# Performance work log

Measured on AMD Instinct MI355X. Metric: run time of the kernel, lower is better.

## Reference

```python
import jax, jax.numpy as jnp
import numpy as np
import math

B_CH = 128   # bottleneck channels (conv1x1 in)
N_CH = 256   # encoder filters (conv1x1 out / linear in)
L = 16       # filter length (linear out); hop = L//2
BATCH = 8
K = 32000    # number of frames
T_ORIGIN = (L // 2) * (K - 1) + L  # 256008


def setup_inputs() -> dict:
    key = jax.random.key(0)
    k1, k2, k3, k4 = jax.random.split(key, 4)
    return {
        "mixture_w": jax.random.normal(k1, (BATCH, N_CH, K), jnp.float32),
        "est_mask": jax.random.normal(k2, (BATCH, B_CH, K), jnp.float32),
        "W_mask": jax.random.normal(k3, (N_CH, B_CH), jnp.float32) * (1.0 / np.sqrt(B_CH)),
        "W_basis": jax.random.normal(k4, (L, N_CH), jnp.float32) * (1.0 / np.sqrt(N_CH)),
        "T_origin": T_ORIGIN,
    }


def overlap_and_add(signal, frame_step):
    # signal: [..., frames, frame_length]
    frames, frame_length = signal.shape[-2], signal.shape[-1]
    sub_len = math.gcd(frame_length, frame_step)
    sub_step = frame_step // sub_len
    spf = frame_length // sub_len  # subframes per frame
    out_size = frame_step * (frames - 1) + frame_length
    out_sub = out_size // sub_len
    sub_sig = signal.reshape(signal.shape[:-2] + (frames * spf, sub_len))
    # scatter index for each subframe (same as torch unfold + index_add_)
    idx = (jnp.arange(frames)[:, None] * sub_step + jnp.arange(spf)[None, :]).reshape(-1)
    res = jnp.zeros(signal.shape[:-2] + (out_sub, sub_len), signal.dtype)
    res = res.at[..., idx, :].add(sub_sig)
    return res.reshape(signal.shape[:-2] + (out_size,))


def reference(mixture_w, est_mask, W_mask, W_basis, T_origin):
    # conv1x1 (bias-free) == channel matmul: [B_CH -> N_CH]
    m = jnp.einsum('nb,gbk->gnk', W_mask, est_mask)   # [batch, N, K]
    x = mixture_w * jax.nn.relu(m)                    # masked encoder output
    # transpose + Linear(N -> L, no bias): [batch, K, L]
    x = jnp.einsum('gnk,ln->gkl', x, W_basis)
    est_source = overlap_and_add(x, L // 2)           # [batch, T_conv]
    pad = T_origin - est_source.shape[-1]
    return jnp.pad(est_source, ((0, 0), (0, pad)))
```

## Files before the change

### kernel.cpp

```cpp
#include <hip/hip_runtime.h>
#include <stdint.h>

#define BATCH 8
#define NCH 256
#define BCH 128
#define KFR 32000
#define TOUT 256008
#define KT 32
#define NCHUNK (KFR / KT)
#define ESTW 64
#define XTW 128
#define LOC_FLOATS (8 * KT + 8)

typedef __attribute__((ext_vector_type(8))) short bf16x8;
typedef __attribute__((ext_vector_type(4))) float f32x4;

__device__ __forceinline__ unsigned short f32_to_bf16(float f) {
    unsigned int u = __builtin_bit_cast(unsigned int, f);
    u += 0x7FFFu + ((u >> 16) & 1u);
    return (unsigned short)(u >> 16);
}
__device__ __forceinline__ unsigned int pack2(float a, float b) {
    return (unsigned int)f32_to_bf16(a) | ((unsigned int)f32_to_bf16(b) << 16);
}
__device__ __forceinline__ int swz(int row, int w) {
    return (((w >> 2) ^ (((row >> 2) & 3) << 1)) << 2) | (w & 3);
}

__global__ void convert_weights(const float* __restrict__ Wm,
                                const float* __restrict__ Wb,
                                unsigned short* __restrict__ wbf) {
    int i = blockIdx.x * 256 + threadIdx.x;
    if (i < NCH * BCH) wbf[i] = f32_to_bf16(Wm[i]);
    if (i < 16 * NCH)  wbf[NCH * BCH + i] = f32_to_bf16(Wb[i]);
}

__global__ __launch_bounds__(256, 4)
void fused_decoder(const float* __restrict__ mix,
                   const float* __restrict__ est,
                   const unsigned short* __restrict__ wbf,
                   float* __restrict__ out) {
    __shared__ __align__(16) unsigned int estd[32 * ESTW];
    __shared__ __align__(16) unsigned int xtd[32 * XTW];
    __shared__ __align__(16) float locout[LOC_FLOATS];

    const int tid = threadIdx.x;
    const int lane = tid & 63;
    const int wv = tid >> 6;
    const int l15 = lane & 15;
    const int lq = lane >> 4;
    const int f4 = tid & 7;
    const int c0 = tid >> 3;

    const int bid = blockIdx.x;
    const int g = bid / NCHUNK;
    const int c = bid % NCHUNK;
    const int k0 = c * KT;

    if (tid < LOC_FLOATS / 4) {
        f32x4 z = {0.f, 0.f, 0.f, 0.f};
        *reinterpret_cast<f32x4*>(locout + 4 * tid) = z;
    }

    const float* eg = est + ((size_t)g * BCH) * KFR + k0;
    const float* mg = mix + ((size_t)g * NCH) * KFR + k0;

    {
        f32x4 e0 = *reinterpret_cast<const f32x4*>(eg + (size_t)(2 * c0) * KFR + 4 * f4);
        f32x4 e1 = *reinterpret_cast<const f32x4*>(eg + (size_t)(2 * c0 + 1) * KFR + 4 * f4);
        f32x4 e2 = *reinterpret_cast<const f32x4*>(eg + (size_t)(2 * c0 + 64) * KFR + 4 * f4);
        f32x4 e3 = *reinterpret_cast<const f32x4*>(eg + (size_t)(2 * c0 + 65) * KFR + 4 * f4);
#pragma unroll
        for (int i = 0; i < 4; ++i) {
            int row = 4 * f4 + i;
            estd[row * ESTW + swz(row, c0)]      = pack2(e0[i], e1[i]);
            estd[row * ESTW + swz(row, c0 + 32)] = pack2(e2[i], e3[i]);
        }
    }
    __syncthreads();

    {
        unsigned short* xts = reinterpret_cast<unsigned short*>(xtd);
#pragma unroll
        for (int nt = 0; nt < 4; ++nt) {
            const int n = 64 * wv + 16 * nt + l15;
            const unsigned short* wr = wbf + n * BCH + 8 * lq;
            bf16x8 w0 = *reinterpret_cast<const bf16x8*>(wr);
            bf16x8 w1 = *reinterpret_cast<const bf16x8*>(wr + 32);
            bf16x8 w2 = *reinterpret_cast<const bf16x8*>(wr + 64);
            bf16x8 w3 = *reinterpret_cast<const bf16x8*>(wr + 96);
#pragma unroll
            for (int ft = 0; ft < 2; ++ft) {
                const int fA = 16 * ft + l15;
                const int sgA = ((l15 >> 2) & 3) << 1;
                const unsigned int* br = estd + fA * ESTW;
                bf16x8 a0 = *reinterpret_cast<const bf16x8*>(br + (((0  + lq) ^ sgA) << 2));
                bf16x8 a1 = *reinterpret_cast<const bf16x8*>(br + (((4  + lq) ^ sgA) << 2));
                bf16x8 a2 = *reinterpret_cast<const bf16x8*>(br + (((8  + lq) ^ sgA) << 2));
                bf16x8 a3 = *reinterpret_cast<const bf16x8*>(br + (((12 + lq) ^ sgA) << 2));
                f32x4 a = {0.f, 0.f, 0.f, 0.f};
                a = __builtin_amdgcn_mfma_f32_16x16x32_bf16(a0, w0, a, 0, 0, 0);
                a = __builtin_amdgcn_mfma_f32_16x16x32_bf16(a1, w1, a, 0, 0, 0);
                a = __builtin_amdgcn_mfma_f32_16x16x32_bf16(a2, w2, a, 0, 0, 0);
                a = __builtin_amdgcn_mfma_f32_16x16x32_bf16(a3, w3, a, 0, 0, 0);
                const int f0 = 16 * ft + 4 * lq;
                f32x4 m = *reinterpret_cast<const f32x4*>(mg + (size_t)n * KFR + f0);
                float x0 = (a[0] > 0.f) ? m[0] * a[0] : 0.f;
                float x1 = (a[1] > 0.f) ? m[1] * a[1] : 0.f;
                float x2 = (a[2] > 0.f) ? m[2] * a[2] : 0.f;
                float x3 = (a[3] > 0.f) ? m[3] * a[3] : 0.f;
                const int swi = (((n >> 3) ^ (lq << 1)) << 2) | ((n >> 1) & 3);
                const int base = f0 * 256 + swi * 2 + (n & 1);
                xts[base]       = f32_to_bf16(x0);
                xts[base + 256] = f32_to_bf16(x1);
                xts[base + 512] = f32_to_bf16(x2);
                xts[base + 768] = f32_to_bf16(x3);
            }
        }
    }
    __syncthreads();

    if (wv < 2) {
        const int f = 16 * wv + l15;
        const int sg = ((f >> 2) & 3) << 1;
        const unsigned int* br = xtd + f * XTW;
        const unsigned short* wb2 = wbf + NCH * BCH + l15 * NCH + 8 * lq;
        f32x4 acc2 = {0.f, 0.f, 0.f, 0.f};
#pragma unroll
        for (int ks = 0; ks < 8; ++ks) {
            bf16x8 a = *reinterpret_cast<const bf16x8*>(wb2 + 32 * ks);
            bf16x8 b = *reinterpret_cast<const bf16x8*>(br + (((4 * ks + lq) ^ sg) << 2));
            acc2 = __builtin_amdgcn_mfma_f32_16x16x32_bf16(a, b, acc2, 0, 0, 0);
        }
        int src = (lane + 31) & 63;
        float p0 = __shfl(acc2[0], src, 64);
        float p1 = __shfl(acc2[1], src, 64);
        float p2 = __shfl(acc2[2], src, 64);
        float p3 = __shfl(acc2[3], src, 64);
        if (lq < 2) {
            int toff = 8 * f + 4 * lq;
            if (l15 == 0) {
                atomicAdd(locout + toff + 0, acc2[0]);
                atomicAdd(locout + toff + 1, acc2[1]);
                atomicAdd(locout + toff + 2, acc2[2]);
                atomicAdd(locout + toff + 3, acc2[3]);
            } else {
                f32x4 s = {acc2[0] + p0, acc2[1] + p1, acc2[2] + p2, acc2[3] + p3};
                *reinterpret_cast<f32x4*>(locout + toff) = s;
            }
        } else if (l15 == 15) {
            int toff = 8 * (16 * wv + 16) + 4 * (lq - 2);
            atomicAdd(locout + toff + 0, acc2[0]);
            atomicAdd(locout + toff + 1, acc2[1]);
            atomicAdd(locout + toff + 2, acc2[2]);
            atomicAdd(locout + toff + 3, acc2[3]);
        }
    }
    __syncthreads();

    if (tid < LOC_FLOATS / 4) {
        float* og = out + (size_t)g * TOUT + (size_t)(8 * KT) * c;
        f32x4 v = *reinterpret_cast<const f32x4*>(locout + 4 * tid);
        if (tid >= 2 && tid < (LOC_FLOATS / 4 - 2)) {
            *reinterpret_cast<f32x4*>(og + 4 * tid) = v;
        } else {
            atomicAdd(og + 4 * tid + 0, v[0]);
            atomicAdd(og + 4 * tid + 1, v[1]);
            atomicAdd(og + 4 * tid + 2, v[2]);
            atomicAdd(og + 4 * tid + 3, v[3]);
        }
    }
}

extern "C" void kernel_launch(void* const* d_in, const int* in_sizes, int n_in,
                              void* d_out, int out_size, void* d_ws, size_t ws_size,
                              hipStream_t stream) {
    const float* mix = (const float*)d_in[0];
    const float* est = (const float*)d_in[1];
    const float* Wm  = (const float*)d_in[2];
    const float* Wb  = (const float*)d_in[3];
    unsigned short* wbf = (unsigned short*)d_ws;

    hipMemsetAsync(d_out, 0, (size_t)out_size * sizeof(float), stream);
    convert_weights<<<128, 256, 0, stream>>>(Wm, Wb, wbf);
    fused_decoder<<<BATCH * NCHUNK, 256, 0, stream>>>(mix, est, wbf, (float*)d_out);
}
```

Baseline: 153.9 us.

## Prefetch mixture loads before first barrier and pad LDS rows

Moves all eight mixture_w global loads for each wave ahead of the est staging barrier so they run alongside the LDS fill and the first GEMM, instead of being issued inside the MFMA loop. Pads the LDS row strides (64→68, 128→132) to change the bank mapping, and relaxes launch bounds from 4 to 2 waves-per-EU to make room for the extra live registers. The cost is higher register pressure and possibly lower occupancy, and the padded strides may interact badly with the existing XOR swizzle.

```diff
diff --git a/kernel.cpp b/kernel.cpp
--- a/kernel.cpp
+++ b/kernel.cpp
@@ -8,8 +8,8 @@
 #define TOUT 256008
 #define KT 32
 #define NCHUNK (KFR / KT)
-#define ESTW 64
-#define XTW 128
+#define ESTW 68
+#define XTW 132
 #define LOC_FLOATS (8 * KT + 8)
 
 typedef __attribute__((ext_vector_type(8))) short bf16x8;
@@ -35,7 +35,39 @@
     if (i < 16 * NCH)  wbf[NCH * BCH + i] = f32_to_bf16(Wb[i]);
 }
 
-__global__ __launch_bounds__(256, 4)
+#define G1(NT, FT, MM) { \
+    const int n = 64 * wv + 16 * (NT) + l15; \
+    const unsigned short* wr = wbf + n * BCH + 8 * lq; \
+    bf16x8 w0 = *reinterpret_cast<const bf16x8*>(wr); \
+    bf16x8 w1 = *reinterpret_cast<const bf16x8*>(wr + 32); \
+    bf16x8 w2 = *reinterpret_cast<const bf16x8*>(wr + 64); \
+    bf16x8 w3 = *reinterpret_cast<const bf16x8*>(wr + 96); \
+    const int fA = 16 * (FT) + l15; \
+    const int sgA = ((l15 >> 2) & 3) << 1; \
+    const unsigned int* br = estd + fA * ESTW; \
+    bf16x8 a0 = *reinterpret_cast<const bf16x8*>(br + (((0  + lq) ^ sgA) << 2)); \
+    bf16x8 a1 = *reinterpret_cast<const bf16x8*>(br + (((4  + lq) ^ sgA) << 2)); \
+    bf16x8 a2 = *reinterpret_cast<const bf16x8*>(br + (((8  + lq) ^ sgA) << 2)); \
+    bf16x8 a3 = *reinterpret_cast<const bf16x8*>(br + (((12 + lq) ^ sgA) << 2)); \
+    f32x4 a = {0.f, 0.f, 0.f, 0.f}; \
+    a = __builtin_amdgcn_mfma_f32_16x16x32_bf16(a0, w0, a, 0, 0, 0); \
+    a = __builtin_amdgcn_mfma_f32_16x16x32_bf16(a1, w1, a, 0, 0, 0); \
+    a = __builtin_amdgcn_mfma_f32_16x16x32_bf16(a2, w2, a, 0, 0, 0); \
+    a = __builtin_amdgcn_mfma_f32_16x16x32_bf16(a3, w3, a, 0, 0, 0); \
+    float x0 = (a[0] > 0.f) ? (MM)[0] * a[0] : 0.f; \
+    float x1 = (a[1] > 0.f) ? (MM)[1] * a[1] : 0.f; \
+    float x2 = (a[2] > 0.f) ? (MM)[2] * a[2] : 0.f; \
+    float x3 = (a[3] > 0.f) ? (MM)[3] * a[3] : 0.f; \
+    const int f0 = 16 * (FT) + 4 * lq; \
+    const int swi = (((n >> 3) ^ (lq << 1)) << 2) | ((n >> 1) & 3); \
+    const int base = f0 * (2 * XTW) + swi * 2 + (n & 1); \
+    xts[base]               = f32_to_bf16(x0); \
+    xts[base + 2 * XTW]     = f32_to_bf16(x1); \
+    xts[base + 4 * XTW]     = f32_to_bf16(x2); \
+    xts[base + 6 * XTW]     = f32_to_bf16(x3); \
+}
+
+__global__ __launch_bounds__(256, 2)
 void fused_decoder(const float* __restrict__ mix,
                    const float* __restrict__ est,
                    const unsigned short* __restrict__ wbf,
@@ -65,58 +97,38 @@
     const float* eg = est + ((size_t)g * BCH) * KFR + k0;
     const float* mg = mix + ((size_t)g * NCH) * KFR + k0;
 
-    {
-        f32x4 e0 = *reinterpret_cast<const f32x4*>(eg + (size_t)(2 * c0) * KFR + 4 * f4);
-        f32x4 e1 = *reinterpret_cast<const f32x4*>(eg + (size_t)(2 * c0 + 1) * KFR + 4 * f4);
-        f32x4 e2 = *reinterpret_cast<const f32x4*>(eg + (size_t)(2 * c0 + 64) * KFR + 4 * f4);
-        f32x4 e3 = *reinterpret_cast<const f32x4*>(eg + (size_t)(2 * c0 + 65) * KFR + 4 * f4);
+    f32x4 e0 = *reinterpret_cast<const f32x4*>(eg + (size_t)(2 * c0) * KFR + 4 * f4);
+    f32x4 e1 = *reinterpret_cast<const f32x4*>(eg + (size_t)(2 * c0 + 1) * KFR + 4 * f4);
+    f32x4 e2 = *reinterpret_cast<const f32x4*>(eg + (size_t)(2 * c0 + 64) * KFR + 4 * f4);
+    f32x4 e3 = *reinterpret_cast<const f32x4*>(eg + (size_t)(2 * c0 + 65) * KFR + 4 * f4);
+    const float* pmb = mg + (size_t)(64 * wv + l15) * KFR + 4 * lq;
+    f32x4 m00 = *reinterpret_cast<const f32x4*>(pmb);
+    f32x4 m01 = *reinterpret_cast<const f32x4*>(pmb + 16);
+    f32x4 m10 = *reinterpret_cast<const f32x4*>(pmb + (size_t)16 * KFR);
+    f32x4 m11 = *reinterpret_cast<const f32x4*>(pmb + (size_t)16 * KFR + 16);
+    f32x4 m20 = *reinterpret_cast<const f32x4*>(pmb + (size_t)32 * KFR);
+    f32x4 m21 = *reinterpret_cast<const f32x4*>(pmb + (size_t)32 * KFR + 16);
+    f32x4 m30 = *reinterpret_cast<const f32x4*>(pmb + (size_t)48 * KFR);
+    f32x4 m31 = *reinterpret_cast<const f32x4*>(pmb + (size_t)48 * KFR + 16);
+
 #pragma unroll
-        for (int i = 0; i < 4; ++i) {
-            int row = 4 * f4 + i;
-            estd[row * ESTW + swz(row, c0)]      = pack2(e0[i], e1[i]);
-            estd[row * ESTW + swz(row, c0 + 32)] = pack2(e2[i], e3[i]);
-        }
+    for (int i = 0; i < 4; ++i) {
+        int row = 4 * f4 + i;
+        estd[row * ESTW + swz(row, c0)]      = pack2(e0[i], e1[i]);
+        estd[row * ESTW + swz(row, c0 + 32)] = pack2(e2[i], e3[i]);
     }
     __syncthreads();
 
     {
         unsigned short* xts = reinterpret_cast<unsigned short*>(xtd);
-#pragma unroll
-        for (int nt = 0; nt < 4; ++nt) {
-            const int n = 64 * wv + 16 * nt + l15;
-            const unsigned short* wr = wbf + n * BCH + 8 * lq;
-            bf16x8 w0 = *reinterpret_cast<const bf16x8*>(wr);
-            bf16x8 w1 = *reinterpret_cast<const bf16x8*>(wr + 32);
-            bf16x8 w2 = *reinterpret_cast<const bf16x8*>(wr + 64);
-            bf16x8 w3 = *reinterpret_cast<const bf16x8*>(wr + 96);
-#pragma unroll
-            for (int ft = 0; ft < 2; ++ft) {
-                const int fA = 16 * ft + l15;
-                const int sgA = ((l15 >> 2) & 3) << 1;
-                const unsigned int* br = estd + fA * ESTW;
-                bf16x8 a0 = *reinterpret_cast<const bf16x8*>(br + (((0  + lq) ^ sgA) << 2));
-                bf16x8 a1 = *reinterpret_cast<const bf16x8*>(br + (((4  + lq) ^ sgA) << 2));
-                bf16x8 a2 = *reinterpret_cast<const bf16x8*>(br + (((8  + lq) ^ sgA) << 2));
-                bf16x8 a3 = *reinterpret_cast<const bf16x8*>(br + (((12 + lq) ^ sgA) << 2));
-                f32x4 a = {0.f, 0.f, 0.f, 0.f};
-                a = __builtin_amdgcn_mfma_f32_16x16x32_bf16(a0, w0, a, 0, 0, 0);
-                a = __builtin_amdgcn_mfma_f32_16x16x32_bf16(a1, w1, a, 0, 0, 0);
-                a = __builtin_amdgcn_mfma_f32_16x16x32_bf16(a2, w2, a, 0, 0, 0);
-                a = __builtin_amdgcn_mfma_f32_16x16x32_bf16(a3, w3, a, 0, 0, 0);
-                const int f0 = 16 * ft + 4 * lq;
-                f32x4 m = *reinterpret_cast<const f32x4*>(mg + (size_t)n * KFR + f0);
-                float x0 = (a[0] > 0.f) ? m[0] * a[0] : 0.f;
-                float x1 = (a[1] > 0.f) ? m[1] * a[1] : 0.f;
-                float x2 = (a[2] > 0.f) ? m[2] * a[2] : 0.f;
-                float x3 = (a[3] > 0.f) ? m[3] * a[3] : 0.f;
-                const int swi = (((n >> 3) ^ (lq << 1)) << 2) | ((n >> 1) & 3);
-                const int base = f0 * 256 + swi * 2 + (n & 1);
-                xts[base]       = f32_to_bf16(x0);
-                xts[base + 256] = f32_to_bf16(x1);
-                xts[base + 512] = f32_to_bf16(x2);
-                xts[base + 768] = f32_to_bf16(x3);
-            }
-        }
+        G1(0, 0, m00)
+        G1(0, 1, m01)
+        G1(1, 0, m10)
+        G1(1, 1, m11)
+        G1(2, 0, m20)
+        G1(2, 1, m21)
+        G1(3, 0, m30)
+        G1(3, 1, m31)
     }
     __syncthreads();
 
```

New measurement: 144.6 us. 1.06x faster.

## Enlarge frame tile and stream mixture channels through LDS with software pipelining

Applied to the files above, without the earlier changes.

Each block now handles 128 frames instead of 32, so there are a quarter as many blocks and fewer boundary atomics. The 256 output channels are processed in eight 32-channel slices. Each slice of mixture data is staged through LDS, and the next slice is prefetched into registers while the current slice's conv and basis MFMAs run. The second GEMM accumulates across slices in registers instead of as a separate phase. In exchange, LDS use per block is higher, occupancy is halved through launch bounds, and there are two barriers per slice.

```diff
diff --git a/kernel.cpp b/kernel.cpp
--- a/kernel.cpp
+++ b/kernel.cpp
@@ -6,10 +6,11 @@
 #define BCH 128
 #define KFR 32000
 #define TOUT 256008
-#define KT 32
+#define KT 128
 #define NCHUNK (KFR / KT)
-#define ESTW 64
-#define XTW 128
+#define ESTW 68
+#define MIXW 132
+#define XTW2 20
 #define LOC_FLOATS (8 * KT + 8)
 
 typedef __attribute__((ext_vector_type(8))) short bf16x8;
@@ -35,139 +36,194 @@
     if (i < 16 * NCH)  wbf[NCH * BCH + i] = f32_to_bf16(Wb[i]);
 }
 
-__global__ __launch_bounds__(256, 4)
+__global__ __launch_bounds__(256, 2)
 void fused_decoder(const float* __restrict__ mix,
                    const float* __restrict__ est,
                    const unsigned short* __restrict__ wbf,
                    float* __restrict__ out) {
-    __shared__ __align__(16) unsigned int estd[32 * ESTW];
-    __shared__ __align__(16) unsigned int xtd[32 * XTW];
-    __shared__ __align__(16) float locout[LOC_FLOATS];
+    __shared__ __align__(16) unsigned int estd[128 * ESTW];
+    __shared__ __align__(16) float        mixs[32 * MIXW];
+    __shared__ __align__(16) unsigned int xtd[128 * XTW2];
+    __shared__ __align__(16) float        locout[1040];
 
     const int tid = threadIdx.x;
     const int lane = tid & 63;
     const int wv = tid >> 6;
     const int l15 = lane & 15;
     const int lq = lane >> 4;
+    const int l31 = lane & 31;
+    const int hi = lane >> 5;
     const int f4 = tid & 7;
     const int c0 = tid >> 3;
 
     const int bid = blockIdx.x;
     const int g = bid / NCHUNK;
     const int c = bid % NCHUNK;
-    const int k0 = c * KT;
-
-    if (tid < LOC_FLOATS / 4) {
+
+    const float* eg = est + ((size_t)g * BCH) * KFR + c * KT;
+    const float* mg = mix + ((size_t)g * NCH) * KFR + c * KT;
+
+    f32x4 e0, e1, e2, e3;
+    {
+        const float* p = eg + (size_t)(2 * c0) * KFR + 4 * f4;
+        e0 = *reinterpret_cast<const f32x4*>(p);
+        e1 = *reinterpret_cast<const f32x4*>(p + (size_t)KFR);
+        e2 = *reinterpret_cast<const f32x4*>(p + (size_t)64 * KFR);
+        e3 = *reinterpret_cast<const f32x4*>(p + (size_t)65 * KFR);
+    }
+    f32x4 mr0, mr1, mr2, mr3;
+    {
+        const float* p = mg + (size_t)(8 * wv + hi) * KFR + 4 * l31;
+        mr0 = *reinterpret_cast<const f32x4*>(p);
+        mr1 = *reinterpret_cast<const f32x4*>(p + (size_t)2 * KFR);
+        mr2 = *reinterpret_cast<const f32x4*>(p + (size_t)4 * KFR);
+        mr3 = *reinterpret_cast<const f32x4*>(p + (size_t)6 * KFR);
+    }
+
+    for (int t2 = tid; t2 < 260; t2 += 256) {
         f32x4 z = {0.f, 0.f, 0.f, 0.f};
-        *reinterpret_cast<f32x4*>(locout + 4 * tid) = z;
-    }
-
-    const float* eg = est + ((size_t)g * BCH) * KFR + k0;
-    const float* mg = mix + ((size_t)g * NCH) * KFR + k0;
-
-    {
-        f32x4 e0 = *reinterpret_cast<const f32x4*>(eg + (size_t)(2 * c0) * KFR + 4 * f4);
-        f32x4 e1 = *reinterpret_cast<const f32x4*>(eg + (size_t)(2 * c0 + 1) * KFR + 4 * f4);
-        f32x4 e2 = *reinterpret_cast<const f32x4*>(eg + (size_t)(2 * c0 + 64) * KFR + 4 * f4);
-        f32x4 e3 = *reinterpret_cast<const f32x4*>(eg + (size_t)(2 * c0 + 65) * KFR + 4 * f4);
+        *reinterpret_cast<f32x4*>(locout + 4 * t2) = z;
+    }
+
+#pragma unroll
+    for (int fb = 0; fb < 4; ++fb) {
 #pragma unroll
         for (int i = 0; i < 4; ++i) {
-            int row = 4 * f4 + i;
+            int row = 32 * fb + 4 * f4 + i;
             estd[row * ESTW + swz(row, c0)]      = pack2(e0[i], e1[i]);
             estd[row * ESTW + swz(row, c0 + 32)] = pack2(e2[i], e3[i]);
         }
+        if (fb < 3) {
+            const float* p = eg + (size_t)(2 * c0) * KFR + 32 * (fb + 1) + 4 * f4;
+            e0 = *reinterpret_cast<const f32x4*>(p);
+            e1 = *reinterpret_cast<const f32x4*>(p + (size_t)KFR);
+            e2 = *reinterpret_cast<const f32x4*>(p + (size_t)64 * KFR);
+            e3 = *reinterpret_cast<const f32x4*>(p + (size_t)65 * KFR);
+        }
+    }
+    {
+        float* d = mixs + (size_t)(8 * wv + hi) * MIXW + 4 * l31;
+        *reinterpret_cast<f32x4*>(d)            = mr0;
+        *reinterpret_cast<f32x4*>(d + 2 * MIXW) = mr1;
+        *reinterpret_cast<f32x4*>(d + 4 * MIXW) = mr2;
+        *reinterpret_cast<f32x4*>(d + 6 * MIXW) = mr3;
     }
     __syncthreads();
 
-    {
-        unsigned short* xts = reinterpret_cast<unsigned short*>(xtd);
-#pragma unroll
-        for (int nt = 0; nt < 4; ++nt) {
-            const int n = 64 * wv + 16 * nt + l15;
-            const unsigned short* wr = wbf + n * BCH + 8 * lq;
-            bf16x8 w0 = *reinterpret_cast<const bf16x8*>(wr);
-            bf16x8 w1 = *reinterpret_cast<const bf16x8*>(wr + 32);
-            bf16x8 w2 = *reinterpret_cast<const bf16x8*>(wr + 64);
-            bf16x8 w3 = *reinterpret_cast<const bf16x8*>(wr + 96);
-#pragma unroll
-            for (int ft = 0; ft < 2; ++ft) {
-                const int fA = 16 * ft + l15;
-                const int sgA = ((l15 >> 2) & 3) << 1;
-                const unsigned int* br = estd + fA * ESTW;
-                bf16x8 a0 = *reinterpret_cast<const bf16x8*>(br + (((0  + lq) ^ sgA) << 2));
-                bf16x8 a1 = *reinterpret_cast<const bf16x8*>(br + (((4  + lq) ^ sgA) << 2));
-                bf16x8 a2 = *reinterpret_cast<const bf16x8*>(br + (((8  + lq) ^ sgA) << 2));
-                bf16x8 a3 = *reinterpret_cast<const bf16x8*>(br + (((12 + lq) ^ sgA) << 2));
+    f32x4 acc2a = {0.f, 0.f, 0.f, 0.f};
+    f32x4 acc2b = {0.f, 0.f, 0.f, 0.f};
+    unsigned short* xts = reinterpret_cast<unsigned short*>(xtd);
+
+    for (int s = 0; s < 8; ++s) {
+#pragma unroll
+        for (int E = 0; E < 2; ++E) {
+            const int ftg = 2 * wv + E;
+            const int fA = 16 * ftg + l15;
+            const int sg = ((l15 >> 2) & 3) << 1;
+            const unsigned int* br = estd + fA * ESTW;
+            bf16x8 a0 = *reinterpret_cast<const bf16x8*>(br + (((0  + lq) ^ sg) << 2));
+            bf16x8 a1 = *reinterpret_cast<const bf16x8*>(br + (((4  + lq) ^ sg) << 2));
+            bf16x8 a2 = *reinterpret_cast<const bf16x8*>(br + (((8  + lq) ^ sg) << 2));
+            bf16x8 a3 = *reinterpret_cast<const bf16x8*>(br + (((12 + lq) ^ sg) << 2));
+#pragma unroll
+            for (int nt = 0; nt < 2; ++nt) {
+                const int nl = 16 * nt + l15;
+                const unsigned short* wr = wbf + (32 * s + nl) * BCH + 8 * lq;
+                bf16x8 w0 = *reinterpret_cast<const bf16x8*>(wr);
+                bf16x8 w1 = *reinterpret_cast<const bf16x8*>(wr + 32);
+                bf16x8 w2 = *reinterpret_cast<const bf16x8*>(wr + 64);
+                bf16x8 w3 = *reinterpret_cast<const bf16x8*>(wr + 96);
                 f32x4 a = {0.f, 0.f, 0.f, 0.f};
                 a = __builtin_amdgcn_mfma_f32_16x16x32_bf16(a0, w0, a, 0, 0, 0);
                 a = __builtin_amdgcn_mfma_f32_16x16x32_bf16(a1, w1, a, 0, 0, 0);
                 a = __builtin_amdgcn_mfma_f32_16x16x32_bf16(a2, w2, a, 0, 0, 0);
                 a = __builtin_amdgcn_mfma_f32_16x16x32_bf16(a3, w3, a, 0, 0, 0);
-                const int f0 = 16 * ft + 4 * lq;
-                f32x4 m = *reinterpret_cast<const f32x4*>(mg + (size_t)n * KFR + f0);
+                const int f0 = 16 * ftg + 4 * lq;
+                const int nl2 = 16 * nt + l15;
+                f32x4 m = *reinterpret_cast<const f32x4*>(mixs + nl2 * MIXW + f0);
                 float x0 = (a[0] > 0.f) ? m[0] * a[0] : 0.f;
                 float x1 = (a[1] > 0.f) ? m[1] * a[1] : 0.f;
                 float x2 = (a[2] > 0.f) ? m[2] * a[2] : 0.f;
                 float x3 = (a[3] > 0.f) ? m[3] * a[3] : 0.f;
-                const int swi = (((n >> 3) ^ (lq << 1)) << 2) | ((n >> 1) & 3);
-                const int base = f0 * 256 + swi * 2 + (n & 1);
-                xts[base]       = f32_to_bf16(x0);
-                xts[base + 256] = f32_to_bf16(x1);
-                xts[base + 512] = f32_to_bf16(x2);
-                xts[base + 768] = f32_to_bf16(x3);
+                const int b = f0 * (2 * XTW2) + nl2;
+                xts[b]                = f32_to_bf16(x0);
+                xts[b + 2 * XTW2]     = f32_to_bf16(x1);
+                xts[b + 4 * XTW2]     = f32_to_bf16(x2);
+                xts[b + 6 * XTW2]     = f32_to_bf16(x3);
             }
         }
-    }
-    __syncthreads();
-
-    if (wv < 2) {
-        const int f = 16 * wv + l15;
-        const int sg = ((f >> 2) & 3) << 1;
-        const unsigned int* br = xtd + f * XTW;
-        const unsigned short* wb2 = wbf + NCH * BCH + l15 * NCH + 8 * lq;
-        f32x4 acc2 = {0.f, 0.f, 0.f, 0.f};
-#pragma unroll
-        for (int ks = 0; ks < 8; ++ks) {
-            bf16x8 a = *reinterpret_cast<const bf16x8*>(wb2 + 32 * ks);
-            bf16x8 b = *reinterpret_cast<const bf16x8*>(br + (((4 * ks + lq) ^ sg) << 2));
-            acc2 = __builtin_amdgcn_mfma_f32_16x16x32_bf16(a, b, acc2, 0, 0, 0);
-        }
-        int src = (lane + 31) & 63;
-        float p0 = __shfl(acc2[0], src, 64);
-        float p1 = __shfl(acc2[1], src, 64);
-        float p2 = __shfl(acc2[2], src, 64);
-        float p3 = __shfl(acc2[3], src, 64);
+        __syncthreads();
+
+        if (s < 7) {
+            const float* p = mg + (size_t)(32 * (s + 1) + 8 * wv + hi) * KFR + 4 * l31;
+            mr0 = *reinterpret_cast<const f32x4*>(p);
+            mr1 = *reinterpret_cast<const f32x4*>(p + (size_t)2 * KFR);
+            mr2 = *reinterpret_cast<const f32x4*>(p + (size_t)4 * KFR);
+            mr3 = *reinterpret_cast<const f32x4*>(p + (size_t)6 * KFR);
+        }
+        {
+            bf16x8 aW = *reinterpret_cast<const bf16x8*>(
+                wbf + NCH * BCH + l15 * NCH + 32 * s + 8 * lq);
+            const unsigned int* x0p = xtd + (size_t)(16 * (2 * wv) + l15) * XTW2 + 4 * lq;
+            const unsigned int* x1p = xtd + (size_t)(16 * (2 * wv + 1) + l15) * XTW2 + 4 * lq;
+            bf16x8 bX0 = *reinterpret_cast<const bf16x8*>(x0p);
+            bf16x8 bX1 = *reinterpret_cast<const bf16x8*>(x1p);
+            acc2a = __builtin_amdgcn_mfma_f32_16x16x32_bf16(aW, bX0, acc2a, 0, 0, 0);
+            acc2b = __builtin_amdgcn_mfma_f32_16x16x32_bf16(aW, bX1, acc2b, 0, 0, 0);
+        }
+        if (s < 7) {
+            float* d = mixs + (size_t)(8 * wv + hi) * MIXW + 4 * l31;
+            *reinterpret_cast<f32x4*>(d)            = mr0;
+            *reinterpret_cast<f32x4*>(d + 2 * MIXW) = mr1;
+            *reinterpret_cast<f32x4*>(d + 4 * MIXW) = mr2;
+            *reinterpret_cast<f32x4*>(d + 6 * MIXW) = mr3;
+        }
+        __syncthreads();
+    }
+
+    const int src = (lane + 31) & 63;
+#pragma unroll
+    for (int E = 0; E < 2; ++E) {
+        const f32x4 a2 = (E == 0) ? acc2a : acc2b;
+        const int ftg = 2 * wv + E;
+        const int f = 16 * ftg + l15;
+        float p0 = __shfl(a2[0], src, 64);
+        float p1 = __shfl(a2[1], src, 64);
+        float p2 = __shfl(a2[2], src, 64);
+        float p3 = __shfl(a2[3], src, 64);
         if (lq < 2) {
             int toff = 8 * f + 4 * lq;
             if (l15 == 0) {
-                atomicAdd(locout + toff + 0, acc2[0]);
-                atomicAdd(locout + toff + 1, acc2[1]);
-                atomicAdd(locout + toff + 2, acc2[2]);
-                atomicAdd(locout + toff + 3, acc2[3]);
+                atomicAdd(locout + toff + 0, a2[0]);
+                atomicAdd(locout + toff + 1, a2[1]);
+                atomicAdd(locout + toff + 2, a2[2]);
+                atomicAdd(locout + toff + 3, a2[3]);
             } else {
-                f32x4 s = {acc2[0] + p0, acc2[1] + p1, acc2[2] + p2, acc2[3] + p3};
-                *reinterpret_cast<f32x4*>(locout + toff) = s;
+                f32x4 sv = {a2[0] + p0, a2[1] + p1, a2[2] + p2, a2[3] + p3};
+                *reinterpret_cast<f32x4*>(locout + toff) = sv;
             }
         } else if (l15 == 15) {
-            int toff = 8 * (16 * wv + 16) + 4 * (lq - 2);
-            atomicAdd(locout + toff + 0, acc2[0]);
-            atomicAdd(locout + toff + 1, acc2[1]);
-            atomicAdd(locout + toff + 2, acc2[2]);
-            atomicAdd(locout + toff + 3, acc2[3]);
+            int toff = 8 * (16 * ftg + 16) + 4 * (lq - 2);
+            atomicAdd(locout + toff + 0, a2[0]);
+            atomicAdd(locout + toff + 1, a2[1]);
+            atomicAdd(locout + toff + 2, a2[2]);
+            atomicAdd(locout + toff + 3, a2[3]);
         }
     }
     __syncthreads();
 
-    if (tid < LOC_FLOATS / 4) {
+    {
         float* og = out + (size_t)g * TOUT + (size_t)(8 * KT) * c;
-        f32x4 v = *reinterpret_cast<const f32x4*>(locout + 4 * tid);
-        if (tid >= 2 && tid < (LOC_FLOATS / 4 - 2)) {
-            *reinterpret_cast<f32x4*>(og + 4 * tid) = v;
-        } else {
-            atomicAdd(og + 4 * tid + 0, v[0]);
-            atomicAdd(og + 4 * tid + 1, v[1]);
-            atomicAdd(og + 4 * tid + 2, v[2]);
-            atomicAdd(og + 4 * tid + 3, v[3]);
+        for (int t2 = tid; t2 < 258; t2 += 256) {
+            f32x4 v = *reinterpret_cast<const f32x4*>(locout + 4 * t2);
+            if (t2 >= 2 && t2 < 256) {
+                *reinterpret_cast<f32x4*>(og + 4 * t2) = v;
+            } else {
+                atomicAdd(og + 4 * t2 + 0, v[0]);
+                atomicAdd(og + 4 * t2 + 1, v[1]);
+                atomicAdd(og + 4 * t2 + 2, v[2]);
+                atomicAdd(og + 4 * t2 + 3, v[3]);
+            }
         }
     }
 }
```

Measured after the change: 180.9 us. +17.6%, slower.
